# Kernel tuning notes

Hardware: AMD Instinct MI355X
Metric: run time of the kernel (lower is better)

Reference implementation:

```python
import jax, jax.numpy as jnp
import numpy as np

BETA = 0.25

def setup_inputs() -> dict:
    key = jax.random.key(0)
    k1, k2 = jax.random.split(key)
    N, D, K = 262144, 64, 512
    encoding = jax.random.normal(k1, (N, D), dtype=jnp.float32)
    # original inits uniform(-1/K, 1/K); scale a normal similarly is fine, but stay faithful:
    weight = jax.random.uniform(k2, (K, D), dtype=jnp.float32, minval=-1.0 / K, maxval=1.0 / K)
    return {"encoding": encoding, "weight": weight}


def reference(encoding, weight):
    # flat view: encoding already [N, D]
    x = encoding  # [N, D]
    # squared euclidean distances; argmin is invariant to sqrt and to ||x||^2 term
    x2 = jnp.sum(x * x, axis=1, keepdims=True)            # [N, 1]
    w2 = jnp.sum(weight * weight, axis=1)                  # [K]
    d2 = x2 - 2.0 * (x @ weight.T) + w2[None, :]           # [N, K]
    idx = jnp.argmin(d2, axis=1)                           # [N]
    quantized = weight[idx]                                # gather == one_hot @ weight, [N, D]

    commitment_loss = jnp.mean((jax.lax.stop_gradient(quantized) - x) ** 2)
    embedding_loss = jnp.mean((quantized - jax.lax.stop_gradient(x)) ** 2)
    vq_loss = commitment_loss * BETA + embedding_loss

    # straight-through estimator
    quantized_st = x + jax.lax.stop_gradient(quantized - x)
    return (idx[:, None], quantized_st, vq_loss)
```

## Files before the change

kernel.cpp:

```cpp
#include <hip/hip_runtime.h>

#define NROWS 262144
#define DDIM  64
#define KCB   512

#define MARGKEY (3u << 17)

#define WS_CNT   0
#define WS_W2P3  1024
#define WS_WHI   4096
#define WS_WMID  69632
#define WS_LIST  135168

typedef __attribute__((ext_vector_type(8))) short short8;
typedef __attribute__((ext_vector_type(4))) float floatx4;
typedef __attribute__((ext_vector_type(2))) unsigned int uintx2;

#if defined(__has_builtin)
#if __has_builtin(__builtin_amdgcn_permlane16_swap) && \
    __has_builtin(__builtin_amdgcn_permlane32_swap)
#define VQ_PLSWAP 1
#endif
#endif

__device__ __forceinline__ unsigned umin2(unsigned a, unsigned b) { return a < b ? a : b; }
__device__ __forceinline__ unsigned umax2(unsigned a, unsigned b) { return a > b ? a : b; }

__device__ __forceinline__ float np_sumsq64(const float* a) {
    float r[8];
#pragma unroll
    for (int j = 0; j < 8; ++j) r[j] = __fmul_rn(a[j], a[j]);
#pragma unroll
    for (int i = 8; i < 64; i += 8) {
#pragma unroll
        for (int j = 0; j < 8; ++j)
            r[j] = __fadd_rn(r[j], __fmul_rn(a[i + j], a[i + j]));
    }
    return __fadd_rn(__fadd_rn(__fadd_rn(r[0], r[1]), __fadd_rn(r[2], r[3])),
                     __fadd_rn(__fadd_rn(r[4], r[5]), __fadd_rn(r[6], r[7])));
}

__device__ __forceinline__ void split2(float e0, float e1, unsigned& hid, unsigned& mid) {
    unsigned u0 = __float_as_uint(e0), u1 = __float_as_uint(e1);
    float r0 = __fsub_rn(e0, __uint_as_float(u0 & 0xFFFF0000u));
    float r1 = __fsub_rn(e1, __uint_as_float(u1 & 0xFFFF0000u));
    hid = (u0 >> 16) | (u1 & 0xFFFF0000u);
    mid = (__float_as_uint(r0) >> 16) | (__float_as_uint(r1) & 0xFFFF0000u);
}

__device__ __forceinline__ void split4(float4 v, uint2& h, uint2& m) {
    unsigned h0, m0, h1, m1;
    split2(v.x, v.y, h0, m0);
    split2(v.z, v.w, h1, m1);
    h = make_uint2(h0, h1);
    m = make_uint2(m0, m1);
}

__device__ __forceinline__ void merge16(unsigned& m1, unsigned& m2) {
#ifdef VQ_PLSWAP
    uintx2 s1 = __builtin_amdgcn_permlane16_swap(m1, m1, false, false);
    uintx2 s2 = __builtin_amdgcn_permlane16_swap(m2, m2, false, false);
    m2 = umin2(umin2(s2[0], s2[1]), umax2(s1[0], s1[1]));
    m1 = umin2(s1[0], s1[1]);
#else
    unsigned o1 = __shfl_xor((int)m1, 16);
    unsigned o2 = __shfl_xor((int)m2, 16);
    m2 = umin2(umin2(m2, o2), umax2(m1, o1));
    m1 = umin2(m1, o1);
#endif
}

__device__ __forceinline__ void merge32(unsigned& m1, unsigned& m2) {
#ifdef VQ_PLSWAP
    uintx2 s1 = __builtin_amdgcn_permlane32_swap(m1, m1, false, false);
    uintx2 s2 = __builtin_amdgcn_permlane32_swap(m2, m2, false, false);
    m2 = umin2(umin2(s2[0], s2[1]), umax2(s1[0], s1[1]));
    m1 = umin2(s1[0], s1[1]);
#else
    unsigned o1 = __shfl_xor((int)m1, 32);
    unsigned o2 = __shfl_xor((int)m2, 32);
    m2 = umin2(umin2(m2, o2), umax2(m1, o1));
    m1 = umin2(m1, o1);
#endif
}

__global__ void vq_prep(const float* __restrict__ w, float* __restrict__ w2p3,
                        unsigned short* __restrict__ whi,
                        unsigned short* __restrict__ wmid) {
    const int k = threadIdx.x;
    float ws[64];
    const float4* wp = (const float4*)(w + (size_t)k * DDIM);
#pragma unroll
    for (int j = 0; j < 16; ++j) {
        float4 v = wp[j];
        ws[4 * j + 0] = v.x; ws[4 * j + 1] = v.y;
        ws[4 * j + 2] = v.z; ws[4 * j + 3] = v.w;
    }
    w2p3[k] = __fadd_rn(np_sumsq64(ws), 3.0f);
#pragma unroll
    for (int d = 0; d < 64; ++d) {
        float v = __fmul_rn(-2.0f, ws[d]);
        unsigned u = __float_as_uint(v);
        whi[k * 64 + d] = (unsigned short)(u >> 16);
        float rem = __fsub_rn(v, __uint_as_float(u & 0xFFFF0000u));
        wmid[k * 64 + d] = (unsigned short)(__float_as_uint(rem) >> 16);
    }
}

__launch_bounds__(512, 4)
__global__ void vq_gemm(const float* __restrict__ x,
                        const unsigned short* __restrict__ whi,
                        const unsigned short* __restrict__ wmid,
                        const float* __restrict__ w2p3g,
                        float* __restrict__ out_idx,
                        unsigned* __restrict__ cnt,
                        unsigned* __restrict__ list, int listcap) {
    const int tid = threadIdx.x;
    const int wave = tid >> 6, lane = tid & 63;
    const int n16 = lane & 15, quad = lane >> 4;

    __shared__ float w2p3s[KCB];
    __shared__ __align__(16) unsigned sbh[2][32 * 36];
    __shared__ __align__(16) unsigned sbm[2][32 * 36];
    __shared__ uint2 mm[8][16][32];

    w2p3s[tid] = w2p3g[tid];

    short8 ah[4][2], am[4][2];
#pragma unroll
    for (int f = 0; f < 4; ++f) {
        const int cw = wave * 64 + f * 16 + n16;
#pragma unroll
        for (int s = 0; s < 2; ++s) {
            ah[f][s] = *(const short8*)(whi + (size_t)cw * 64 + s * 32 + quad * 8);
            am[f][s] = *(const short8*)(wmid + (size_t)cw * 64 + s * 32 + quad * 8);
        }
    }

    const int r0 = blockIdx.x * 512;
    const int srow = tid >> 4, sc4 = tid & 15;
    {
        float4 v = *(const float4*)(x + (size_t)(r0 + srow) * DDIM + 4 * sc4);
        uint2 h, m; split4(v, h, m);
        *(uint2*)&sbh[0][srow * 36 + 2 * sc4] = h;
        *(uint2*)&sbm[0][srow * 36 + 2 * sc4] = m;
    }
    __syncthreads();

    const unsigned cwq = (unsigned)(wave * 64 + quad * 4);

    for (int it = 0; it < 16; ++it) {
        const int p = it & 1;
        float4 pre;
        if (it < 15)
            pre = *(const float4*)(x + (size_t)(r0 + (it + 1) * 32 + srow) * DDIM + 4 * sc4);

#pragma unroll
        for (int sub = 0; sub < 2; ++sub) {
            const int rb = (sub * 16 + n16) * 36;
            short8 b_h0 = *(const short8*)&sbh[p][rb + quad * 4];
            short8 b_h1 = *(const short8*)&sbh[p][rb + 16 + quad * 4];
            short8 b_m0 = *(const short8*)&sbm[p][rb + quad * 4];
            short8 b_m1 = *(const short8*)&sbm[p][rb + 16 + quad * 4];

            floatx4 acc[4];
#pragma unroll
            for (int f = 0; f < 4; ++f)
                acc[f] = *(const floatx4*)&w2p3s[wave * 64 + f * 16 + quad * 4];
#pragma unroll
            for (int f = 0; f < 4; ++f) {
                acc[f] = __builtin_amdgcn_mfma_f32_16x16x32_bf16(ah[f][0], b_h0, acc[f], 0, 0, 0);
                acc[f] = __builtin_amdgcn_mfma_f32_16x16x32_bf16(ah[f][0], b_m0, acc[f], 0, 0, 0);
                acc[f] = __builtin_amdgcn_mfma_f32_16x16x32_bf16(am[f][0], b_h0, acc[f], 0, 0, 0);
                acc[f] = __builtin_amdgcn_mfma_f32_16x16x32_bf16(ah[f][1], b_h1, acc[f], 0, 0, 0);
                acc[f] = __builtin_amdgcn_mfma_f32_16x16x32_bf16(ah[f][1], b_m1, acc[f], 0, 0, 0);
                acc[f] = __builtin_amdgcn_mfma_f32_16x16x32_bf16(am[f][1], b_h1, acc[f], 0, 0, 0);
            }

            unsigned p1[4], p2[4];
#pragma unroll
            for (int f = 0; f < 4; ++f) {
                unsigned k0 = (__float_as_uint(acc[f][0]) << 9) + (cwq + (unsigned)(f * 16 + 0));
                unsigned k1 = (__float_as_uint(acc[f][1]) << 9) + (cwq + (unsigned)(f * 16 + 1));
                unsigned k2 = (__float_as_uint(acc[f][2]) << 9) + (cwq + (unsigned)(f * 16 + 2));
                unsigned k3 = (__float_as_uint(acc[f][3]) << 9) + (cwq + (unsigned)(f * 16 + 3));
                unsigned lo01 = umin2(k0, k1), hi01 = umax2(k0, k1);
                unsigned lo23 = umin2(k2, k3), hi23 = umax2(k2, k3);
                p1[f] = umin2(lo01, lo23);
                p2[f] = umin2(umax2(lo01, lo23), umin2(hi01, hi23));
            }
            unsigned q1a = umin2(p1[0], p1[1]);
            unsigned q2a = umin2(umax2(p1[0], p1[1]), umin2(p2[0], p2[1]));
            unsigned q1b = umin2(p1[2], p1[3]);
            unsigned q2b = umin2(umax2(p1[2], p1[3]), umin2(p2[2], p2[3]));
            unsigned m1 = umin2(q1a, q1b);
            unsigned m2 = umin2(umax2(q1a, q1b), umin2(q2a, q2b));

            merge16(m1, m2);
            merge32(m1, m2);
            if (lane < 16) mm[wave][it][sub * 16 + n16] = make_uint2(m1, m2);
        }

        if (it < 15) {
            uint2 h, m; split4(pre, h, m);
            *(uint2*)&sbh[p ^ 1][srow * 36 + 2 * sc4] = h;
            *(uint2*)&sbm[p ^ 1][srow * 36 + 2 * sc4] = m;
        }
        __syncthreads();
    }

    unsigned a1 = 0xFFFFFFFFu, a2 = 0xFFFFFFFFu;
#pragma unroll
    for (int wv = 0; wv < 8; ++wv) {
        uint2 v = mm[wv][tid >> 5][tid & 31];
        a2 = umin2(umin2(a2, v.y), umax2(a1, v.x));
        a1 = umin2(a1, v.x);
    }
    out_idx[r0 + tid] = (float)(a1 & 511u);
    bool flag = (a2 - a1 < MARGKEY);
    unsigned long long mask = __ballot(flag);
    int nw = __popcll(mask);
    unsigned base = 0;
    if (lane == 0 && nw) base = atomicAdd(cnt, (unsigned)nw);
    base = (unsigned)__shfl((int)base, 0);
    if (flag) {
        unsigned pos = base + (unsigned)__popcll(mask & ((1ull << lane) - 1ull));
        if ((int)pos < listcap) list[pos] = (unsigned)(r0 + tid);
    }
}

__launch_bounds__(512, 4)
__global__ void vq_recheck(const float* __restrict__ x,
                           const float* __restrict__ w,
                           const unsigned* __restrict__ cnt,
                           const unsigned* __restrict__ list, int listcap,
                           float* __restrict__ out_idx) {
    const int tid = threadIdx.x;
    unsigned total = *cnt;
    if (total > (unsigned)listcap) total = (unsigned)listcap;
    const unsigned nb = (total + 15) >> 4;
    if (blockIdx.x >= nb) return;

    float wl[64];
    {
        const float4* wp = (const float4*)(w + (size_t)tid * DDIM);
#pragma unroll
        for (int j = 0; j < 16; ++j) {
            float4 v = wp[j];
            wl[4 * j + 0] = v.x; wl[4 * j + 1] = v.y;
            wl[4 * j + 2] = v.z; wl[4 * j + 3] = v.w;
        }
    }
    const float w2l = np_sumsq64(wl);

    __shared__ float d2tile[16][KCB];
    __shared__ int rowbuf[16];
    __shared__ float x2buf[16];

    for (unsigned batch = blockIdx.x; batch < nb; batch += gridDim.x) {
        if (tid < 16) {
            unsigned li = batch * 16 + (unsigned)tid;
            rowbuf[tid] = (li < total) ? (int)list[li] : -1;
        }
        __syncthreads();

        if (tid < 128) {
            const int rl = tid >> 3, j = tid & 7;
            int row = rowbuf[rl]; if (row < 0) row = 0;
            const float* xr = x + (size_t)row * DDIM;
            float a0 = xr[j];
            float r = __fmul_rn(a0, a0);
#pragma unroll
            for (int i = 1; i < 8; ++i) {
                float ai = xr[8 * i + j];
                r = __fadd_rn(r, __fmul_rn(ai, ai));
            }
            float s1 = __fadd_rn(r,  __shfl_xor(r, 1));
            float s2 = __fadd_rn(s1, __shfl_xor(s1, 2));
            float s4 = __fadd_rn(s2, __shfl_xor(s2, 4));
            if (j == 0) x2buf[rl] = s4;
        }
        __syncthreads();

        for (int g = 0; g < 16; g += 4) {
            int ra = rowbuf[g + 0]; if (ra < 0) ra = 0;
            int rb = rowbuf[g + 1]; if (rb < 0) rb = 0;
            int rc = rowbuf[g + 2]; if (rc < 0) rc = 0;
            int rd = rowbuf[g + 3]; if (rd < 0) rd = 0;
            const float* xr0 = x + (size_t)ra * DDIM;
            const float* xr1 = x + (size_t)rb * DDIM;
            const float* xr2 = x + (size_t)rc * DDIM;
            const float* xr3 = x + (size_t)rd * DDIM;
            float m0 = 0.f, m1 = 0.f, m2 = 0.f, m3 = 0.f;
#pragma unroll
            for (int jb = 0; jb < 16; ++jb) {
                float4 a0 = *(const float4*)(xr0 + 4 * jb);
                float4 a1 = *(const float4*)(xr1 + 4 * jb);
                float4 a2 = *(const float4*)(xr2 + 4 * jb);
                float4 a3 = *(const float4*)(xr3 + 4 * jb);
                m0 = __fmaf_rn(a0.x, wl[4 * jb + 0], m0);
                m0 = __fmaf_rn(a0.y, wl[4 * jb + 1], m0);
                m0 = __fmaf_rn(a0.z, wl[4 * jb + 2], m0);
                m0 = __fmaf_rn(a0.w, wl[4 * jb + 3], m0);
                m1 = __fmaf_rn(a1.x, wl[4 * jb + 0], m1);
                m1 = __fmaf_rn(a1.y, wl[4 * jb + 1], m1);
                m1 = __fmaf_rn(a1.z, wl[4 * jb + 2], m1);
                m1 = __fmaf_rn(a1.w, wl[4 * jb + 3], m1);
                m2 = __fmaf_rn(a2.x, wl[4 * jb + 0], m2);
                m2 = __fmaf_rn(a2.y, wl[4 * jb + 1], m2);
                m2 = __fmaf_rn(a2.z, wl[4 * jb + 2], m2);
                m2 = __fmaf_rn(a2.w, wl[4 * jb + 3], m2);
                m3 = __fmaf_rn(a3.x, wl[4 * jb + 0], m3);
                m3 = __fmaf_rn(a3.y, wl[4 * jb + 1], m3);
                m3 = __fmaf_rn(a3.z, wl[4 * jb + 2], m3);
                m3 = __fmaf_rn(a3.w, wl[4 * jb + 3], m3);
            }
            float X0 = x2buf[g + 0], X1 = x2buf[g + 1];
            float X2 = x2buf[g + 2], X3 = x2buf[g + 3];
            d2tile[g + 0][tid] = __fadd_rn(__fsub_rn(X0, __fmul_rn(2.0f, m0)), w2l);
            d2tile[g + 1][tid] = __fadd_rn(__fsub_rn(X1, __fmul_rn(2.0f, m1)), w2l);
            d2tile[g + 2][tid] = __fadd_rn(__fsub_rn(X2, __fmul_rn(2.0f, m2)), w2l);
            d2tile[g + 3][tid] = __fadd_rn(__fsub_rn(X3, __fmul_rn(2.0f, m3)), w2l);
        }
        __syncthreads();

        {
            const int rl  = tid >> 5;
            const int sub = tid & 31;
            float bv = d2tile[rl][sub];
            int   bi = sub;
#pragma unroll
            for (int i = 1; i < 16; ++i) {
                int cc = sub + 32 * i;
                float v = d2tile[rl][cc];
                if (v < bv) { bv = v; bi = cc; }
            }
#pragma unroll
            for (int s = 1; s < 32; s <<= 1) {
                float ov = __shfl_xor(bv, s);
                int   oi = __shfl_xor(bi, s);
                if (ov < bv || (ov == bv && oi < bi)) { bv = ov; bi = oi; }
            }
            if (sub == 0 && rowbuf[rl] >= 0) out_idx[rowbuf[rl]] = (float)bi;
        }
        __syncthreads();
    }
}

__launch_bounds__(256)
__global__ void vq_epilogue(const float* __restrict__ x,
                            const float* __restrict__ w,
                            const float* __restrict__ out_idx_f,
                            float* __restrict__ out_q,
                            float* __restrict__ out_loss) {
    const int row  = blockIdx.x * blockDim.x + threadIdx.x;
    const int bidx = (int)out_idx_f[row];

    const float4* xp = (const float4*)(x + (size_t)row * DDIM);
    const float4* wq = (const float4*)(w + (size_t)bidx * DDIM);
    float4* qo = (float4*)(out_q + (size_t)row * DDIM);
    float ls = 0.0f;
#pragma unroll
    for (int j = 0; j < 16; ++j) {
        float4 xv = xp[j];
        float4 wv = wq[j];
        float e0 = __fsub_rn(wv.x, xv.x), e1 = __fsub_rn(wv.y, xv.y);
        float e2 = __fsub_rn(wv.z, xv.z), e3 = __fsub_rn(wv.w, xv.w);
        ls = fmaf(e0, e0, ls); ls = fmaf(e1, e1, ls);
        ls = fmaf(e2, e2, ls); ls = fmaf(e3, e3, ls);
        float4 q;
        q.x = __fadd_rn(xv.x, e0); q.y = __fadd_rn(xv.y, e1);
        q.z = __fadd_rn(xv.z, e2); q.w = __fadd_rn(xv.w, e3);
        qo[j] = q;
    }
#pragma unroll
    for (int off = 32; off > 0; off >>= 1) ls += __shfl_down(ls, off);
    __shared__ float red[4];
    const int lane = threadIdx.x & 63;
    const int wid  = threadIdx.x >> 6;
    if (lane == 0) red[wid] = ls;
    __syncthreads();
    if (threadIdx.x == 0) {
        float t = (red[0] + red[1]) + (red[2] + red[3]);
        atomicAdd(out_loss, t * (1.25f / (float)(NROWS * DDIM)));
    }
}

extern "C" void kernel_launch(void* const* d_in, const int* in_sizes, int n_in,
                              void* d_out, int out_size, void* d_ws, size_t ws_size,
                              hipStream_t stream) {
    const float* x = (const float*)d_in[0];
    const float* w = (const float*)d_in[1];

    float* out      = (float*)d_out;
    float* out_idx  = out;
    float* out_q    = out + (size_t)NROWS;
    float* out_loss = out + (size_t)NROWS + (size_t)NROWS * DDIM;

    char* ws = (char*)d_ws;
    unsigned* cnt  = (unsigned*)(ws + WS_CNT);
    float* w2p3    = (float*)(ws + WS_W2P3);
    unsigned short* whi  = (unsigned short*)(ws + WS_WHI);
    unsigned short* wmid = (unsigned short*)(ws + WS_WMID);
    unsigned* list = (unsigned*)(ws + WS_LIST);
    long cap = ((long)ws_size - WS_LIST) / 4;
    int listcap = cap > 0 ? (cap > NROWS ? NROWS : (int)cap) : 0;

    hipMemsetAsync(out_loss, 0, sizeof(float), stream);
    hipMemsetAsync(cnt, 0, sizeof(unsigned), stream);

    vq_prep<<<1, 512, 0, stream>>>(w, w2p3, whi, wmid);
    vq_gemm<<<NROWS / 512, 512, 0, stream>>>(x, whi, wmid, w2p3, out_idx, cnt, list, listcap);
    vq_recheck<<<256, 512, 0, stream>>>(x, w, cnt, list, listcap, out_idx);
    vq_epilogue<<<NROWS / 256, 256, 0, stream>>>(x, w, out_idx, out_q, out_loss);
}
```

Baseline: 255.6 us.

## Load x directly into MFMA fragments, drop LDS staging and memsets

The GEMM kernel no longer stages x through double-buffered LDS with a per-iteration barrier. Each lane now loads its MFMA B-fragment rows straight from global memory and splits them into bf16 hi/mid in registers. The two hipMemsetAsync calls move into the prep kernel, which also uses vectorized short8 stores and a 2x256 launch. This removes LDS traffic, 16 barriers per block and two host-side memset launches. In exchange it loses the explicit prefetch overlap, and each lane's global loads are less coalesced (row-strided 32-byte chunks).

```diff
diff --git a/kernel.cpp b/kernel.cpp
--- a/kernel.cpp
+++ b/kernel.cpp
@@ -48,12 +48,13 @@
     mid = (__float_as_uint(r0) >> 16) | (__float_as_uint(r1) & 0xFFFF0000u);
 }
 
-__device__ __forceinline__ void split4(float4 v, uint2& h, uint2& m) {
-    unsigned h0, m0, h1, m1;
-    split2(v.x, v.y, h0, m0);
-    split2(v.z, v.w, h1, m1);
-    h = make_uint2(h0, h1);
-    m = make_uint2(m0, m1);
+__device__ __forceinline__ void build8(float4 a, float4 b, short8& hi, short8& mi) {
+    union { unsigned d[4]; short8 s; } H, M;
+    split2(a.x, a.y, H.d[0], M.d[0]);
+    split2(a.z, a.w, H.d[1], M.d[1]);
+    split2(b.x, b.y, H.d[2], M.d[2]);
+    split2(b.z, b.w, H.d[3], M.d[3]);
+    hi = H.s; mi = M.s;
 }
 
 __device__ __forceinline__ void merge16(unsigned& m1, unsigned& m2) {
@@ -86,8 +87,10 @@
 
 __global__ void vq_prep(const float* __restrict__ w, float* __restrict__ w2p3,
                         unsigned short* __restrict__ whi,
-                        unsigned short* __restrict__ wmid) {
-    const int k = threadIdx.x;
+                        unsigned short* __restrict__ wmid,
+                        unsigned* __restrict__ cnt, float* __restrict__ loss) {
+    const int k = blockIdx.x * blockDim.x + threadIdx.x;
+    if (k == 0) { *cnt = 0u; *loss = 0.0f; }
     float ws[64];
     const float4* wp = (const float4*)(w + (size_t)k * DDIM);
 #pragma unroll
@@ -98,12 +101,16 @@
     }
     w2p3[k] = __fadd_rn(np_sumsq64(ws), 3.0f);
 #pragma unroll
-    for (int d = 0; d < 64; ++d) {
-        float v = __fmul_rn(-2.0f, ws[d]);
-        unsigned u = __float_as_uint(v);
-        whi[k * 64 + d] = (unsigned short)(u >> 16);
-        float rem = __fsub_rn(v, __uint_as_float(u & 0xFFFF0000u));
-        wmid[k * 64 + d] = (unsigned short)(__float_as_uint(rem) >> 16);
+    for (int j = 0; j < 8; ++j) {
+        union { unsigned d[4]; short8 s; } H, M;
+#pragma unroll
+        for (int t = 0; t < 4; ++t) {
+            float v0 = __fmul_rn(-2.0f, ws[8 * j + 2 * t]);
+            float v1 = __fmul_rn(-2.0f, ws[8 * j + 2 * t + 1]);
+            split2(v0, v1, H.d[t], M.d[t]);
+        }
+        *(short8*)(whi  + (size_t)k * 64 + 8 * j) = H.s;
+        *(short8*)(wmid + (size_t)k * 64 + 8 * j) = M.s;
     }
 }
 
@@ -120,8 +127,6 @@
     const int n16 = lane & 15, quad = lane >> 4;
 
     __shared__ float w2p3s[KCB];
-    __shared__ __align__(16) unsigned sbh[2][32 * 36];
-    __shared__ __align__(16) unsigned sbm[2][32 * 36];
     __shared__ uint2 mm[8][16][32];
 
     w2p3s[tid] = w2p3g[tid];
@@ -137,31 +142,33 @@
         }
     }
 
+    __syncthreads();
+
     const int r0 = blockIdx.x * 512;
-    const int srow = tid >> 4, sc4 = tid & 15;
-    {
-        float4 v = *(const float4*)(x + (size_t)(r0 + srow) * DDIM + 4 * sc4);
-        uint2 h, m; split4(v, h, m);
-        *(uint2*)&sbh[0][srow * 36 + 2 * sc4] = h;
-        *(uint2*)&sbm[0][srow * 36 + 2 * sc4] = m;
-    }
-    __syncthreads();
-
     const unsigned cwq = (unsigned)(wave * 64 + quad * 4);
 
     for (int it = 0; it < 16; ++it) {
-        const int p = it & 1;
-        float4 pre;
-        if (it < 15)
-            pre = *(const float4*)(x + (size_t)(r0 + (it + 1) * 32 + srow) * DDIM + 4 * sc4);
+        const float* xr0 = x + (size_t)(r0 + it * 32 + n16) * DDIM + quad * 8;
+        const float* xr1 = xr0 + 16 * DDIM;
+        float4 a00 = *(const float4*)(xr0);
+        float4 a01 = *(const float4*)(xr0 + 4);
+        float4 a02 = *(const float4*)(xr0 + 32);
+        float4 a03 = *(const float4*)(xr0 + 36);
+        float4 a10 = *(const float4*)(xr1);
+        float4 a11 = *(const float4*)(xr1 + 4);
+        float4 a12 = *(const float4*)(xr1 + 32);
+        float4 a13 = *(const float4*)(xr1 + 36);
 
 #pragma unroll
         for (int sub = 0; sub < 2; ++sub) {
-            const int rb = (sub * 16 + n16) * 36;
-            short8 b_h0 = *(const short8*)&sbh[p][rb + quad * 4];
-            short8 b_h1 = *(const short8*)&sbh[p][rb + 16 + quad * 4];
-            short8 b_m0 = *(const short8*)&sbm[p][rb + quad * 4];
-            short8 b_m1 = *(const short8*)&sbm[p][rb + 16 + quad * 4];
+            short8 b_h0, b_m0, b_h1, b_m1;
+            if (sub == 0) {
+                build8(a00, a01, b_h0, b_m0);
+                build8(a02, a03, b_h1, b_m1);
+            } else {
+                build8(a10, a11, b_h0, b_m0);
+                build8(a12, a13, b_h1, b_m1);
+            }
 
             floatx4 acc[4];
 #pragma unroll
@@ -200,14 +207,8 @@
             merge32(m1, m2);
             if (lane < 16) mm[wave][it][sub * 16 + n16] = make_uint2(m1, m2);
         }
-
-        if (it < 15) {
-            uint2 h, m; split4(pre, h, m);
-            *(uint2*)&sbh[p ^ 1][srow * 36 + 2 * sc4] = h;
-            *(uint2*)&sbm[p ^ 1][srow * 36 + 2 * sc4] = m;
-        }
-        __syncthreads();
-    }
+    }
+    __syncthreads();
 
     unsigned a1 = 0xFFFFFFFFu, a2 = 0xFFFFFFFFu;
 #pragma unroll
@@ -406,10 +407,7 @@
     long cap = ((long)ws_size - WS_LIST) / 4;
     int listcap = cap > 0 ? (cap > NROWS ? NROWS : (int)cap) : 0;
 
-    hipMemsetAsync(out_loss, 0, sizeof(float), stream);
-    hipMemsetAsync(cnt, 0, sizeof(unsigned), stream);
-
-    vq_prep<<<1, 512, 0, stream>>>(w, w2p3, whi, wmid);
+    vq_prep<<<2, 256, 0, stream>>>(w, w2p3, whi, wmid, cnt, out_loss);
     vq_gemm<<<NROWS / 512, 512, 0, stream>>>(x, whi, wmid, w2p3, out_idx, cnt, list, listcap);
     vq_recheck<<<256, 512, 0, stream>>>(x, w, cnt, list, listcap, out_idx);
     vq_epilogue<<<NROWS / 256, 256, 0, stream>>>(x, w, out_idx, out_q, out_loss);
```

Result: slower. 275.1 us (+7.6%).

## Split codebook across two 256-thread blocks and merge top-2 in separate kernel

Applied to the files above, without the earlier changes.

The GEMM kernel now uses 256-thread blocks that each handle half of the codebook (256 codes) for 256 rows, writing per-half top-2 keys to a scratch buffer aliased onto the quantized output. A new merge kernel combines the two halves, writes the index and appends ambiguous rows to the recheck list. The memsets are folded into the prep kernel, which also vectorises its bf16 split stores. This aims to improve scheduling and occupancy, at the cost of an extra launch, a global round-trip of 4 MB, and each row tile of x being loaded twice.

```diff
diff --git a/kernel.cpp b/kernel.cpp
--- a/kernel.cpp
+++ b/kernel.cpp
@@ -86,8 +86,10 @@
 
 __global__ void vq_prep(const float* __restrict__ w, float* __restrict__ w2p3,
                         unsigned short* __restrict__ whi,
-                        unsigned short* __restrict__ wmid) {
-    const int k = threadIdx.x;
+                        unsigned short* __restrict__ wmid,
+                        unsigned* __restrict__ cnt, float* __restrict__ loss) {
+    const int k = blockIdx.x * blockDim.x + threadIdx.x;
+    if (k == 0) { *cnt = 0u; *loss = 0.0f; }
     float ws[64];
     const float4* wp = (const float4*)(w + (size_t)k * DDIM);
 #pragma unroll
@@ -98,38 +100,42 @@
     }
     w2p3[k] = __fadd_rn(np_sumsq64(ws), 3.0f);
 #pragma unroll
-    for (int d = 0; d < 64; ++d) {
-        float v = __fmul_rn(-2.0f, ws[d]);
-        unsigned u = __float_as_uint(v);
-        whi[k * 64 + d] = (unsigned short)(u >> 16);
-        float rem = __fsub_rn(v, __uint_as_float(u & 0xFFFF0000u));
-        wmid[k * 64 + d] = (unsigned short)(__float_as_uint(rem) >> 16);
-    }
-}
-
-__launch_bounds__(512, 4)
+    for (int j = 0; j < 8; ++j) {
+        union { unsigned d[4]; short8 s; } H, M;
+#pragma unroll
+        for (int t = 0; t < 4; ++t) {
+            float v0 = __fmul_rn(-2.0f, ws[8 * j + 2 * t]);
+            float v1 = __fmul_rn(-2.0f, ws[8 * j + 2 * t + 1]);
+            split2(v0, v1, H.d[t], M.d[t]);
+        }
+        *(short8*)(whi  + (size_t)k * 64 + 8 * j) = H.s;
+        *(short8*)(wmid + (size_t)k * 64 + 8 * j) = M.s;
+    }
+}
+
+__launch_bounds__(256, 4)
 __global__ void vq_gemm(const float* __restrict__ x,
                         const unsigned short* __restrict__ whi,
                         const unsigned short* __restrict__ wmid,
                         const float* __restrict__ w2p3g,
-                        float* __restrict__ out_idx,
-                        unsigned* __restrict__ cnt,
-                        unsigned* __restrict__ list, int listcap) {
+                        uint2* __restrict__ mmg) {
     const int tid = threadIdx.x;
     const int wave = tid >> 6, lane = tid & 63;
     const int n16 = lane & 15, quad = lane >> 4;
-
-    __shared__ float w2p3s[KCB];
+    const int half = blockIdx.x & 1;
+    const int r0 = (blockIdx.x >> 1) * 256;
+
+    __shared__ float w2p3s[256];
     __shared__ __align__(16) unsigned sbh[2][32 * 36];
     __shared__ __align__(16) unsigned sbm[2][32 * 36];
-    __shared__ uint2 mm[8][16][32];
-
-    w2p3s[tid] = w2p3g[tid];
+    __shared__ uint2 mm[4][8][32];
+
+    w2p3s[tid] = w2p3g[half * 256 + tid];
 
     short8 ah[4][2], am[4][2];
 #pragma unroll
     for (int f = 0; f < 4; ++f) {
-        const int cw = wave * 64 + f * 16 + n16;
+        const int cw = half * 256 + wave * 64 + f * 16 + n16;
 #pragma unroll
         for (int s = 0; s < 2; ++s) {
             ah[f][s] = *(const short8*)(whi + (size_t)cw * 64 + s * 32 + quad * 8);
@@ -137,23 +143,29 @@
         }
     }
 
-    const int r0 = blockIdx.x * 512;
     const int srow = tid >> 4, sc4 = tid & 15;
     {
-        float4 v = *(const float4*)(x + (size_t)(r0 + srow) * DDIM + 4 * sc4);
-        uint2 h, m; split4(v, h, m);
+        float4 v0 = *(const float4*)(x + (size_t)(r0 + srow) * DDIM + 4 * sc4);
+        float4 v1 = *(const float4*)(x + (size_t)(r0 + srow + 16) * DDIM + 4 * sc4);
+        uint2 h, m;
+        split4(v0, h, m);
         *(uint2*)&sbh[0][srow * 36 + 2 * sc4] = h;
         *(uint2*)&sbm[0][srow * 36 + 2 * sc4] = m;
+        split4(v1, h, m);
+        *(uint2*)&sbh[0][(srow + 16) * 36 + 2 * sc4] = h;
+        *(uint2*)&sbm[0][(srow + 16) * 36 + 2 * sc4] = m;
     }
     __syncthreads();
 
-    const unsigned cwq = (unsigned)(wave * 64 + quad * 4);
-
-    for (int it = 0; it < 16; ++it) {
+    const unsigned cwq = (unsigned)(half * 256 + wave * 64 + quad * 4);
+
+    for (int it = 0; it < 8; ++it) {
         const int p = it & 1;
-        float4 pre;
-        if (it < 15)
-            pre = *(const float4*)(x + (size_t)(r0 + (it + 1) * 32 + srow) * DDIM + 4 * sc4);
+        float4 pre0, pre1;
+        if (it < 7) {
+            pre0 = *(const float4*)(x + (size_t)(r0 + (it + 1) * 32 + srow) * DDIM + 4 * sc4);
+            pre1 = *(const float4*)(x + (size_t)(r0 + (it + 1) * 32 + srow + 16) * DDIM + 4 * sc4);
+        }
 
 #pragma unroll
         for (int sub = 0; sub < 2; ++sub) {
@@ -201,22 +213,40 @@
             if (lane < 16) mm[wave][it][sub * 16 + n16] = make_uint2(m1, m2);
         }
 
-        if (it < 15) {
-            uint2 h, m; split4(pre, h, m);
+        if (it < 7) {
+            uint2 h, m;
+            split4(pre0, h, m);
             *(uint2*)&sbh[p ^ 1][srow * 36 + 2 * sc4] = h;
             *(uint2*)&sbm[p ^ 1][srow * 36 + 2 * sc4] = m;
+            split4(pre1, h, m);
+            *(uint2*)&sbh[p ^ 1][(srow + 16) * 36 + 2 * sc4] = h;
+            *(uint2*)&sbm[p ^ 1][(srow + 16) * 36 + 2 * sc4] = m;
         }
         __syncthreads();
     }
 
     unsigned a1 = 0xFFFFFFFFu, a2 = 0xFFFFFFFFu;
 #pragma unroll
-    for (int wv = 0; wv < 8; ++wv) {
+    for (int wv = 0; wv < 4; ++wv) {
         uint2 v = mm[wv][tid >> 5][tid & 31];
         a2 = umin2(umin2(a2, v.y), umax2(a1, v.x));
         a1 = umin2(a1, v.x);
     }
-    out_idx[r0 + tid] = (float)(a1 & 511u);
+    mmg[(size_t)half * NROWS + (r0 + tid)] = make_uint2(a1, a2);
+}
+
+__launch_bounds__(256)
+__global__ void vq_merge(const uint2* __restrict__ mmg,
+                         float* __restrict__ out_idx,
+                         unsigned* __restrict__ cnt,
+                         unsigned* __restrict__ list, int listcap) {
+    const int row = blockIdx.x * 256 + threadIdx.x;
+    const int lane = threadIdx.x & 63;
+    uint2 v0 = mmg[row];
+    uint2 v1 = mmg[(size_t)NROWS + row];
+    unsigned a1 = umin2(v0.x, v1.x);
+    unsigned a2 = umin2(umax2(v0.x, v1.x), umin2(v0.y, v1.y));
+    out_idx[row] = (float)(a1 & 511u);
     bool flag = (a2 - a1 < MARGKEY);
     unsigned long long mask = __ballot(flag);
     int nw = __popcll(mask);
@@ -225,7 +255,7 @@
     base = (unsigned)__shfl((int)base, 0);
     if (flag) {
         unsigned pos = base + (unsigned)__popcll(mask & ((1ull << lane) - 1ull));
-        if ((int)pos < listcap) list[pos] = (unsigned)(r0 + tid);
+        if ((int)pos < listcap) list[pos] = (unsigned)row;
     }
 }
 
@@ -397,6 +427,8 @@
     float* out_q    = out + (size_t)NROWS;
     float* out_loss = out + (size_t)NROWS + (size_t)NROWS * DDIM;
 
+    uint2* mmg = (uint2*)out_q;
+
     char* ws = (char*)d_ws;
     unsigned* cnt  = (unsigned*)(ws + WS_CNT);
     float* w2p3    = (float*)(ws + WS_W2P3);
@@ -406,11 +438,9 @@
     long cap = ((long)ws_size - WS_LIST) / 4;
     int listcap = cap > 0 ? (cap > NROWS ? NROWS : (int)cap) : 0;
 
-    hipMemsetAsync(out_loss, 0, sizeof(float), stream);
-    hipMemsetAsync(cnt, 0, sizeof(unsigned), stream);
-
-    vq_prep<<<1, 512, 0, stream>>>(w, w2p3, whi, wmid);
-    vq_gemm<<<NROWS / 512, 512, 0, stream>>>(x, whi, wmid, w2p3, out_idx, cnt, list, listcap);
+    vq_prep<<<2, 256, 0, stream>>>(w, w2p3, whi, wmid, cnt, out_loss);
+    vq_gemm<<<2048, 256, 0, stream>>>(x, whi, wmid, w2p3, mmg);
+    vq_merge<<<NROWS / 256, 256, 0, stream>>>(mmg, out_idx, cnt, list, listcap);
     vq_recheck<<<256, 512, 0, stream>>>(x, w, cnt, list, listcap, out_idx);
     vq_epilogue<<<NROWS / 256, 256, 0, stream>>>(x, w, out_idx, out_q, out_loss);
 }
```

Result: slower. 285.3 us (+11.6%).
